# Kernel tuning notes

Hardware: AMD Instinct MI355X
Metric: run time of the kernel (lower is better)

The kernel has to match this reference:

```python
import jax, jax.numpy as jnp
import numpy as np

N_ = 512   # batch / num users
M_ = 254   # num UAV nodes -> size S = M_ + 2 = 256
D_ = 2     # coordinate dim
H_ = 128   # pointer-net hidden dim


def setup_inputs() -> dict:
    key = jax.random.key(0)
    ks = jax.random.split(key, 7)
    s = 0.1
    return {
        "outputs": jax.random.normal(ks[0], (2 * N_ + M_, D_), dtype=jnp.float32),
        "W_embed": jax.random.normal(ks[1], (D_, H_), dtype=jnp.float32) * s,
        "b_embed": jnp.zeros((H_,), jnp.float32),
        "lstm_Wi": jax.random.normal(ks[2], (H_, 4 * H_), dtype=jnp.float32) * s,
        "lstm_Wh": jax.random.normal(ks[3], (H_, 4 * H_), dtype=jnp.float32) * s,
        "lstm_b": jnp.zeros((4 * H_,), jnp.float32),
        "att_W1": jax.random.normal(ks[4], (H_, H_), dtype=jnp.float32) * s,
        "att_W2": jax.random.normal(ks[5], (H_, H_), dtype=jnp.float32) * s,
        "att_v": jax.random.normal(ks[6], (H_,), dtype=jnp.float32) * s,
        "N": N_,
    }


def _rgnn_loss(outputs, W_embed, b_embed, lstm_Wi, lstm_Wh, lstm_b,
               att_W1, att_W2, att_v, N):
    D = outputs.shape[1]
    H = W_embed.shape[1]
    M = outputs.shape[0] - 2 * N
    users_src = outputs[:N][:, None, :]                         # (B,1,D)
    users_dst = outputs[N:2 * N][:, None, :]                    # (B,1,D)
    uav_nodes = jnp.broadcast_to(outputs[2 * N:][None, :, :], (N, M, D))
    uav_graph = jnp.concatenate([users_src, uav_nodes, users_dst], axis=1)  # (B,S,D)
    B, S = uav_graph.shape[0], uav_graph.shape[1]
    NEG = jnp.float32(-np.inf)

    # pointer-net: node embeddings and step-independent attention projection
    e_all = uav_graph @ W_embed + b_embed                       # (B,S,H)
    W1e = jnp.einsum('bsh,hk->bsk', e_all, att_W1)              # (B,S,H)
    rows = jnp.arange(B)

    mask0 = jnp.zeros((B, S), jnp.float32).at[:, 0].set(NEG)
    x0 = uav_graph[:, 0, :]                                     # start at src
    carry0 = (x0, x0,
              jnp.zeros((B, H), jnp.float32), jnp.zeros((B, H), jnp.float32),
              mask0, jnp.zeros((B,), jnp.float32))

    def step(carry, k):
        x, Y0, h, c, mask, max_dist = carry
        # dst node blocked only at step 0, re-opened afterwards
        mask = mask.at[:, -1].set(jnp.where(k == 0, NEG, 0.0))
        # LSTM cell on embedded current node
        e_x = x @ W_embed + b_embed                             # (B,H)
        gates = e_x @ lstm_Wi + h @ lstm_Wh + lstm_b            # (B,4H)
        i, f, g, o = jnp.split(gates, 4, axis=1)
        c = jax.nn.sigmoid(f) * c + jax.nn.sigmoid(i) * jnp.tanh(g)
        h = jax.nn.sigmoid(o) * jnp.tanh(c)
        # additive attention pointer logits
        q = h @ att_W2                                          # (B,H)
        logits = jnp.tanh(W1e + q[:, None, :]) @ att_v + mask   # (B,S)
        logits = jax.lax.stop_gradient(logits)                  # output.detach()
        idx = jnp.argmax(logits, axis=1)                        # (B,)
        Y1 = uav_graph[rows, idx]                               # (B,D)
        dist = jnp.sqrt(jnp.sum((Y1 - Y0) ** 2, axis=1) + 1e-12)
        max_dist = jnp.maximum(max_dist, dist)
        mask = mask.at[rows, idx].add(NEG)
        mask = jnp.where((idx == S)[:, None], NEG, mask)
        return (Y1, Y1, h, c, mask, max_dist), None

    (_, _, _, _, _, max_dist), _ = jax.lax.scan(step, carry0, jnp.arange(S))
    return max_dist.mean()


def reference(outputs, W_embed, b_embed, lstm_Wi, lstm_Wh, lstm_b,
              att_W1, att_W2, att_v, N):
    return _rgnn_loss(outputs, W_embed, b_embed, lstm_Wi, lstm_Wh, lstm_b,
                      att_W1, att_W2, att_v, N)
```

## Files before the change

kernel.cpp:

```cpp
#include <hip/hip_runtime.h>
#include <math.h>

#define NB   512
#define MM   254
#define SS   256
#define HH   128
#define RTOT 1278
#define NBLK 256

#define C2   2.885390081777927f
#define C1   1.442695040888963f

__device__ __forceinline__ float rcpf(float x)  { return __builtin_amdgcn_rcpf(x); }
__device__ __forceinline__ float exp2f_(float x){ return __builtin_amdgcn_exp2f(x); }
__device__ __forceinline__ float sigm2(float x) { return rcpf(1.0f + exp2f_(-C1 * x)); }
__device__ __forceinline__ float tanh2(float x) { return 1.0f - 2.0f * rcpf(1.0f + exp2f_(C2 * x)); }

__global__ __launch_bounds__(512) void coef_k(
    const float* __restrict__ Wemb, const float* __restrict__ bemb,
    const float* __restrict__ Wi, const float* __restrict__ W1,
    const float* __restrict__ lb, float* __restrict__ coef)
{
  int j = threadIdx.x;
  float a = 0.f, b = 0.f, c = 0.f;
#pragma unroll 8
  for (int h = 0; h < HH; ++h) {
    float w = Wi[(size_t)h * 512 + j];
    a = fmaf(Wemb[h], w, a);
    b = fmaf(Wemb[HH + h], w, b);
    c = fmaf(bemb[h], w, c);
  }
  coef[j] = a; coef[512 + j] = b; coef[1024 + j] = c + lb[j];
  if (j < HH) {
    float a1 = 0.f, b1 = 0.f, c1 = 0.f;
#pragma unroll 8
    for (int h = 0; h < HH; ++h) {
      float w = W1[(size_t)h * HH + j];
      a1 = fmaf(Wemb[h], w, a1);
      b1 = fmaf(Wemb[HH + h], w, b1);
      c1 = fmaf(bemb[h], w, c1);
    }
    coef[1536 + j] = C2 * a1; coef[1664 + j] = C2 * b1; coef[1792 + j] = C2 * c1;
  }
}

__global__ __launch_bounds__(128) void transpose_k(
    const float* __restrict__ Wh, const float* __restrict__ W2,
    float* __restrict__ WhT, float* __restrict__ W2T)
{
  int bidx = blockIdx.x;
  int k = threadIdx.x;
  if (bidx < 512) WhT[(size_t)bidx * 128 + k] = Wh[(size_t)k * 512 + bidx];
  else {
    int j = bidx - 512;
    W2T[(size_t)j * 128 + k] = W2[(size_t)k * 128 + j];
  }
}

__global__ __attribute__((amdgpu_waves_per_eu(4, 4)))
__launch_bounds__(1024) void decode_k(
    const float* __restrict__ outputs, const float* __restrict__ WhT,
    const float* __restrict__ Wh, const float* __restrict__ W2T,
    const float* __restrict__ av, const float* __restrict__ coef,
    float* __restrict__ maxd_out)
{
  const int t = threadIdx.x;
  const int bid = blockIdx.x;

  __shared__ float WhL[64][512];
  __shared__ float posU[2 * MM];
  __shared__ float dstS[2][2];
  __shared__ float curP[2][2];
  __shared__ __align__(16) float hS[2][HH];
  __shared__ __align__(16) float qC[2][HH];
  __shared__ float C1sS[HH];
  __shared__ __align__(16) float A1sS[HH], B1sS[HH], vS2[HH];
  __shared__ __align__(16) float AiS[512], BiS[512], CiS[512];
  __shared__ float pS[2][2][512];
  __shared__ float lp[2][4][SS];
  __shared__ int   actS[2][254];
  __shared__ int   cntS[2];

  const int gh  = (t >> 5) & 1;
  const int gj  = ((t >> 6) << 5) | (t & 31);
  const int cg  = t >> 9;
  const int cj  = (t >> 2) & 127;
  const int ckq = t & 3;
  const int lg  = t >> 9;
  const int lhq = (t >> 7) & 3;
  const int lu  = t & 127;

  for (int i = t; i < 64 * 512; i += 1024) ((float*)WhL)[i] = Wh[64 * 512 + i];
  for (int i = t; i < 2 * MM; i += 1024)   posU[i] = outputs[4 * NB + i];
  if (t < HH) {
    C1sS[t] = coef[1792 + t];
    A1sS[t] = coef[1536 + t];
    B1sS[t] = coef[1664 + t];
    vS2[t]  = -2.0f * av[t];
  }
  if (t < 512) { AiS[t] = coef[t]; BiS[t] = coef[512 + t]; CiS[t] = coef[1024 + t]; }
  if (t < 256) { int gg = t >> 7, j = t & 127; hS[gg][j] = 0.f; }
  if (t < 254) actS[0][t] = t + 1;
  else if (t >= 512 && t < 766) actS[1][t - 512] = t - 511;
  if (t == 0) {
    cntS[0] = 254;
    dstS[0][0] = outputs[2 * (NB + bid)]; dstS[0][1] = outputs[2 * (NB + bid) + 1];
    curP[0][0] = outputs[2 * bid];        curP[0][1] = outputs[2 * bid + 1];
  }
  if (t == 512) {
    cntS[1] = 254;
    dstS[1][0] = outputs[2 * (NB + bid + NBLK)];
    dstS[1][1] = outputs[2 * (NB + bid + NBLK) + 1];
    curP[1][0] = outputs[2 * (bid + NBLK)];
    curP[1][1] = outputs[2 * (bid + NBLK) + 1];
  }
  __syncthreads();

  float px = 0.f, py = 0.f, md = 0.f;
  if (t == 0)   { px = curP[0][0]; py = curP[0][1]; }
  if (t == 512) { px = curP[1][0]; py = curP[1][1]; }

  float creg = 0.f;

  for (int k = 0; k < SS; ++k) {
    {
      const float4* wg4 = (const float4*)(WhT + (size_t)gj * 128 + gh * 32);
      const float*  wl  = &WhL[gh * 32][gj];
      const float4* hb0g = (const float4*)(&hS[0][gh * 32]);
      const float4* hb1g = (const float4*)(&hS[1][gh * 32]);
      const float4* hb0l = (const float4*)(&hS[0][64 + gh * 32]);
      const float4* hb1l = (const float4*)(&hS[1][64 + gh * 32]);
      float a0G = 0.f, a1G = 0.f, a0L = 0.f, a1L = 0.f;
      float4 wb[4];
#pragma unroll
      for (int i = 0; i < 4; ++i) wb[i] = wg4[i];
#pragma unroll
      for (int i = 0; i < 4; ++i) {
        float4 h0 = hb0l[i], h1 = hb1l[i];
        float wa = wl[(size_t)(4 * i) * 512];
        float wbv = wl[(size_t)(4 * i + 1) * 512];
        float wc = wl[(size_t)(4 * i + 2) * 512];
        float wd = wl[(size_t)(4 * i + 3) * 512];
        a0L = fmaf(h0.x, wa, a0L); a0L = fmaf(h0.y, wbv, a0L);
        a0L = fmaf(h0.z, wc, a0L); a0L = fmaf(h0.w, wd, a0L);
        a1L = fmaf(h1.x, wa, a1L); a1L = fmaf(h1.y, wbv, a1L);
        a1L = fmaf(h1.z, wc, a1L); a1L = fmaf(h1.w, wd, a1L);
      }
#pragma unroll
      for (int i = 0; i < 4; ++i) {
        float4 h0 = hb0g[i], h1 = hb1g[i], w = wb[i];
        a0G = fmaf(h0.x, w.x, a0G); a0G = fmaf(h0.y, w.y, a0G);
        a0G = fmaf(h0.z, w.z, a0G); a0G = fmaf(h0.w, w.w, a0G);
        a1G = fmaf(h1.x, w.x, a1G); a1G = fmaf(h1.y, w.y, a1G);
        a1G = fmaf(h1.z, w.z, a1G); a1G = fmaf(h1.w, w.w, a1G);
      }
#pragma unroll
      for (int i = 0; i < 4; ++i) wb[i] = wg4[4 + i];
#pragma unroll
      for (int i = 4; i < 8; ++i) {
        float4 h0 = hb0l[i], h1 = hb1l[i];
        float wa = wl[(size_t)(4 * i) * 512];
        float wbv = wl[(size_t)(4 * i + 1) * 512];
        float wc = wl[(size_t)(4 * i + 2) * 512];
        float wd = wl[(size_t)(4 * i + 3) * 512];
        a0L = fmaf(h0.x, wa, a0L); a0L = fmaf(h0.y, wbv, a0L);
        a0L = fmaf(h0.z, wc, a0L); a0L = fmaf(h0.w, wd, a0L);
        a1L = fmaf(h1.x, wa, a1L); a1L = fmaf(h1.y, wbv, a1L);
        a1L = fmaf(h1.z, wc, a1L); a1L = fmaf(h1.w, wd, a1L);
      }
#pragma unroll
      for (int i = 0; i < 4; ++i) {
        float4 h0 = hb0g[4 + i], h1 = hb1g[4 + i], w = wb[i];
        a0G = fmaf(h0.x, w.x, a0G); a0G = fmaf(h0.y, w.y, a0G);
        a0G = fmaf(h0.z, w.z, a0G); a0G = fmaf(h0.w, w.w, a0G);
        a1G = fmaf(h1.x, w.x, a1G); a1G = fmaf(h1.y, w.y, a1G);
        a1G = fmaf(h1.z, w.z, a1G); a1G = fmaf(h1.w, w.w, a1G);
      }
      pS[0][gh][gj] = a0G + a0L;
      pS[1][gh][gj] = a1G + a1L;
    }
    __syncthreads();

    if (t < 256) {
      int g = t >> 7, jj = t & 127;
      float pxc = curP[g][0], pyc = curP[g][1];
      float ei = fmaf(pxc, AiS[jj],       fmaf(pyc, BiS[jj],       CiS[jj]))       + (pS[g][0][jj]       + pS[g][1][jj]);
      float ef = fmaf(pxc, AiS[128 + jj], fmaf(pyc, BiS[128 + jj], CiS[128 + jj])) + (pS[g][0][128 + jj] + pS[g][1][128 + jj]);
      float eg2 = fmaf(pxc, AiS[256 + jj], fmaf(pyc, BiS[256 + jj], CiS[256 + jj])) + (pS[g][0][256 + jj] + pS[g][1][256 + jj]);
      float eo = fmaf(pxc, AiS[384 + jj], fmaf(pyc, BiS[384 + jj], CiS[384 + jj])) + (pS[g][0][384 + jj] + pS[g][1][384 + jj]);
      float iv = sigm2(ei), fv = sigm2(ef), gv = tanh2(eg2), ov = sigm2(eo);
      float cn = fv * creg + iv * gv;
      creg = cn;
      hS[g][jj] = ov * tanh2(cn);
    }
    __syncthreads();

    {
      const float4* w4 = (const float4*)(W2T + (size_t)cj * 128 + ckq * 32);
      const float4* h4 = (const float4*)(&hS[cg][ckq * 32]);
      float p0 = 0.f, p1 = 0.f;
#pragma unroll
      for (int i = 0; i < 8; ++i) {
        float4 w = w4[i], h = h4[i];
        p0 = fmaf(h.x, w.x, p0); p1 = fmaf(h.y, w.y, p1);
        p0 = fmaf(h.z, w.z, p0); p1 = fmaf(h.w, w.w, p1);
      }
      float p = p0 + p1;
      p += __shfl_xor(p, 1);
      p += __shfl_xor(p, 2);
      if (ckq == 0) qC[cg][cj] = fmaf(C2, p, C1sS[cj]);
    }
    __syncthreads();

    {
      int cnt = cntS[lg];
      int cntEff = cnt + (k > 0 ? 1 : 0);
      int u0 = lu, u1 = lu + 128;
      bool e0 = u0 < cntEff, e1 = u1 < cntEff;
      float px0 = 0.f, py0 = 0.f, px1 = 0.f, py1 = 0.f;
      if (e0) {
        int s0 = (u0 == cnt) ? 255 : actS[lg][u0];
        if (s0 == 255) { px0 = dstS[lg][0]; py0 = dstS[lg][1]; }
        else           { px0 = posU[2 * (s0 - 1)]; py0 = posU[2 * (s0 - 1) + 1]; }
      }
      if (e1) {
        int s1 = (u1 == cnt) ? 255 : actS[lg][u1];
        if (s1 == 255) { px1 = dstS[lg][0]; py1 = dstS[lg][1]; }
        else           { px1 = posU[2 * (s1 - 1)]; py1 = posU[2 * (s1 - 1) + 1]; }
      }
      const float4* a14 = (const float4*)(&A1sS[lhq * 32]);
      const float4* b14 = (const float4*)(&B1sS[lhq * 32]);
      const float4* qc4 = (const float4*)(&qC[lg][lhq * 32]);
      const float4* vv4 = (const float4*)(&vS2[lhq * 32]);
      float c00 = 0.f, c01 = 0.f, c10 = 0.f, c11 = 0.f;
#pragma unroll 4
      for (int i = 0; i < 8; ++i) {
        float4 a = a14[i], b = b14[i], qc = qc4[i], v = vv4[i];
        if (e0) {
          c00 = fmaf(v.x, rcpf(1.0f + exp2f_(fmaf(px0, a.x, fmaf(py0, b.x, qc.x)))), c00);
          c01 = fmaf(v.y, rcpf(1.0f + exp2f_(fmaf(px0, a.y, fmaf(py0, b.y, qc.y)))), c01);
          c00 = fmaf(v.z, rcpf(1.0f + exp2f_(fmaf(px0, a.z, fmaf(py0, b.z, qc.z)))), c00);
          c01 = fmaf(v.w, rcpf(1.0f + exp2f_(fmaf(px0, a.w, fmaf(py0, b.w, qc.w)))), c01);
        }
        if (e1) {
          c10 = fmaf(v.x, rcpf(1.0f + exp2f_(fmaf(px1, a.x, fmaf(py1, b.x, qc.x)))), c10);
          c11 = fmaf(v.y, rcpf(1.0f + exp2f_(fmaf(px1, a.y, fmaf(py1, b.y, qc.y)))), c11);
          c10 = fmaf(v.z, rcpf(1.0f + exp2f_(fmaf(px1, a.z, fmaf(py1, b.z, qc.z)))), c10);
          c11 = fmaf(v.w, rcpf(1.0f + exp2f_(fmaf(px1, a.w, fmaf(py1, b.w, qc.w)))), c11);
        }
      }
      if (e0) lp[lg][lhq][u0] = c00 + c01;
      if (e1) lp[lg][lhq][u1] = c10 + c11;
    }
    __syncthreads();

    if ((t < 64) || (t >= 512 && t < 576)) {
      int g = t >> 9;
      int lane = t & 63;
      int cnt = cntS[g];
      int cntEff = cnt + (k > 0 ? 1 : 0);
      float val = -INFINITY;
      unsigned key = 0xFFFFFFFFu;
#pragma unroll 2
      for (int c = 0; c < 4; ++c) {
        int u = lane + 64 * c;
        if (u < cntEff) {
          float v2 = (lp[g][0][u] + lp[g][1][u]) + (lp[g][2][u] + lp[g][3][u]);
          int s = (u == cnt) ? 255 : actS[g][u];
          unsigned k2 = ((unsigned)s << 16) | (unsigned)u;
          if (v2 > val || (v2 == val && k2 < key)) { val = v2; key = k2; }
        }
      }
#pragma unroll
      for (int off = 1; off < 64; off <<= 1) {
        float v2 = __shfl_xor(val, off);
        unsigned k2 = __shfl_xor(key, off);
        if (v2 > val || (v2 == val && k2 < key)) { val = v2; key = k2; }
      }
      if (lane == 0) {
        int s   = (int)(key >> 16);
        int pos = (int)(key & 0xFFFFu);
        float nx, ny;
        if (s == 255) { nx = dstS[g][0]; ny = dstS[g][1]; }
        else          { nx = posU[2 * (s - 1)]; ny = posU[2 * (s - 1) + 1]; }
        float dx = nx - px, dy = ny - py;
        float d = sqrtf(dx * dx + dy * dy + 1e-12f);
        if (d > md) md = d;
        px = nx; py = ny;
        curP[g][0] = nx; curP[g][1] = ny;
        if (s != 255) { actS[g][pos] = actS[g][cnt - 1]; cntS[g] = cnt - 1; }
      }
    }
    __syncthreads();
  }

  if (t == 0)   maxd_out[bid] = md;
  if (t == 512) maxd_out[bid + NBLK] = md;
}

__global__ __launch_bounds__(512) void reduce_k(const float* __restrict__ maxd,
                                               float* __restrict__ out)
{
  __shared__ float s[512];
  int t = threadIdx.x;
  s[t] = maxd[t];
  __syncthreads();
  for (int off = 256; off > 0; off >>= 1) {
    if (t < off) s[t] += s[t + off];
    __syncthreads();
  }
  if (t == 0) out[0] = s[0] * (1.0f / 512.0f);
}

extern "C" void kernel_launch(void* const* d_in, const int* in_sizes, int n_in,
                              void* d_out, int out_size, void* d_ws, size_t ws_size,
                              hipStream_t stream) {
  const float* outputs = (const float*)d_in[0];
  const float* Wemb    = (const float*)d_in[1];
  const float* bemb    = (const float*)d_in[2];
  const float* Wi      = (const float*)d_in[3];
  const float* Wh      = (const float*)d_in[4];
  const float* lb      = (const float*)d_in[5];
  const float* W1      = (const float*)d_in[6];
  const float* W2      = (const float*)d_in[7];
  const float* av      = (const float*)d_in[8];

  float* ws   = (float*)d_ws;
  float* coef = ws;
  float* WhT  = coef + 2048;
  float* W2T  = WhT + (size_t)512 * 128;
  float* maxd = W2T + (size_t)128 * 128;

  hipLaunchKernelGGL(coef_k, dim3(1), dim3(512), 0, stream,
                     Wemb, bemb, Wi, W1, lb, coef);
  hipLaunchKernelGGL(transpose_k, dim3(640), dim3(128), 0, stream, Wh, W2, WhT, W2T);
  hipLaunchKernelGGL(decode_k, dim3(NBLK), dim3(1024), 0, stream,
                     outputs, WhT, Wh, W2T, av, coef, maxd);
  hipLaunchKernelGGL(reduce_k, dim3(1), dim3(512), 0, stream, maxd, (float*)d_out);
}
```

Before: 2.122 ms.

## Stagger two per-block teams by two phases to overlap decode stages

The decode kernel now gives each 512-thread half of the block its own batch element, so each half computes its full gate matvec instead of the two halves splitting the work across both elements. The second team starts two phases behind the first, so the five phases (gate matvec, LSTM update, query projection, attention logits, argmax) of the two teams run in a staggered pipeline. This is meant to mix different instruction types on the CU at the same moment and avoid whole-block idle time in the lightly occupied phases. In exchange there are two extra stage barriers, per-thread dot products are twice as long, and each team reads the full Wh matrix on its own.

After: 7.943 ms. 3.74x slower.

```diff
diff --git a/kernel.cpp b/kernel.cpp
--- a/kernel.cpp
+++ b/kernel.cpp
@@ -66,6 +66,9 @@
 {
   const int t = threadIdx.x;
   const int bid = blockIdx.x;
+  const int team  = t >> 9;
+  const int local = t & 511;
+  const int g = team;
 
   __shared__ float WhL[64][512];
   __shared__ float posU[2 * MM];
@@ -76,19 +79,15 @@
   __shared__ float C1sS[HH];
   __shared__ __align__(16) float A1sS[HH], B1sS[HH], vS2[HH];
   __shared__ __align__(16) float AiS[512], BiS[512], CiS[512];
-  __shared__ float pS[2][2][512];
+  __shared__ __align__(16) float gS[2][512];
   __shared__ float lp[2][4][SS];
   __shared__ int   actS[2][254];
   __shared__ int   cntS[2];
 
-  const int gh  = (t >> 5) & 1;
-  const int gj  = ((t >> 6) << 5) | (t & 31);
-  const int cg  = t >> 9;
-  const int cj  = (t >> 2) & 127;
-  const int ckq = t & 3;
-  const int lg  = t >> 9;
-  const int lhq = (t >> 7) & 3;
-  const int lu  = t & 127;
+  const int cj  = (local >> 2) & 127;
+  const int ckq = local & 3;
+  const int lhq = (local >> 7) & 3;
+  const int lu  = local & 127;
 
   for (int i = t; i < 64 * 512; i += 1024) ((float*)WhL)[i] = Wh[64 * 512 + i];
   for (int i = t; i < 2 * MM; i += 1024)   posU[i] = outputs[4 * NB + i];
@@ -117,185 +116,161 @@
   __syncthreads();
 
   float px = 0.f, py = 0.f, md = 0.f;
-  if (t == 0)   { px = curP[0][0]; py = curP[0][1]; }
-  if (t == 512) { px = curP[1][0]; py = curP[1][1]; }
+  if (local == 0) {
+    int b = bid + (g << 8);
+    px = outputs[2 * b]; py = outputs[2 * b + 1];
+  }
 
   float creg = 0.f;
 
-  for (int k = 0; k < SS; ++k) {
-    {
-      const float4* wg4 = (const float4*)(WhT + (size_t)gj * 128 + gh * 32);
-      const float*  wl  = &WhL[gh * 32][gj];
-      const float4* hb0g = (const float4*)(&hS[0][gh * 32]);
-      const float4* hb1g = (const float4*)(&hS[1][gh * 32]);
-      const float4* hb0l = (const float4*)(&hS[0][64 + gh * 32]);
-      const float4* hb1l = (const float4*)(&hS[1][64 + gh * 32]);
-      float a0G = 0.f, a1G = 0.f, a0L = 0.f, a1L = 0.f;
-      float4 wb[4];
-#pragma unroll
-      for (int i = 0; i < 4; ++i) wb[i] = wg4[i];
-#pragma unroll
-      for (int i = 0; i < 4; ++i) {
-        float4 h0 = hb0l[i], h1 = hb1l[i];
-        float wa = wl[(size_t)(4 * i) * 512];
-        float wbv = wl[(size_t)(4 * i + 1) * 512];
-        float wc = wl[(size_t)(4 * i + 2) * 512];
-        float wd = wl[(size_t)(4 * i + 3) * 512];
-        a0L = fmaf(h0.x, wa, a0L); a0L = fmaf(h0.y, wbv, a0L);
-        a0L = fmaf(h0.z, wc, a0L); a0L = fmaf(h0.w, wd, a0L);
-        a1L = fmaf(h1.x, wa, a1L); a1L = fmaf(h1.y, wbv, a1L);
-        a1L = fmaf(h1.z, wc, a1L); a1L = fmaf(h1.w, wd, a1L);
-      }
-#pragma unroll
-      for (int i = 0; i < 4; ++i) {
-        float4 h0 = hb0g[i], h1 = hb1g[i], w = wb[i];
-        a0G = fmaf(h0.x, w.x, a0G); a0G = fmaf(h0.y, w.y, a0G);
-        a0G = fmaf(h0.z, w.z, a0G); a0G = fmaf(h0.w, w.w, a0G);
-        a1G = fmaf(h1.x, w.x, a1G); a1G = fmaf(h1.y, w.y, a1G);
-        a1G = fmaf(h1.z, w.z, a1G); a1G = fmaf(h1.w, w.w, a1G);
-      }
-#pragma unroll
-      for (int i = 0; i < 4; ++i) wb[i] = wg4[4 + i];
-#pragma unroll
-      for (int i = 4; i < 8; ++i) {
-        float4 h0 = hb0l[i], h1 = hb1l[i];
-        float wa = wl[(size_t)(4 * i) * 512];
-        float wbv = wl[(size_t)(4 * i + 1) * 512];
-        float wc = wl[(size_t)(4 * i + 2) * 512];
-        float wd = wl[(size_t)(4 * i + 3) * 512];
-        a0L = fmaf(h0.x, wa, a0L); a0L = fmaf(h0.y, wbv, a0L);
-        a0L = fmaf(h0.z, wc, a0L); a0L = fmaf(h0.w, wd, a0L);
-        a1L = fmaf(h1.x, wa, a1L); a1L = fmaf(h1.y, wbv, a1L);
-        a1L = fmaf(h1.z, wc, a1L); a1L = fmaf(h1.w, wd, a1L);
-      }
-#pragma unroll
-      for (int i = 0; i < 4; ++i) {
-        float4 h0 = hb0g[4 + i], h1 = hb1g[4 + i], w = wb[i];
-        a0G = fmaf(h0.x, w.x, a0G); a0G = fmaf(h0.y, w.y, a0G);
-        a0G = fmaf(h0.z, w.z, a0G); a0G = fmaf(h0.w, w.w, a0G);
-        a1G = fmaf(h1.x, w.x, a1G); a1G = fmaf(h1.y, w.y, a1G);
-        a1G = fmaf(h1.z, w.z, a1G); a1G = fmaf(h1.w, w.w, a1G);
-      }
-      pS[0][gh][gj] = a0G + a0L;
-      pS[1][gh][gj] = a1G + a1L;
-    }
-    __syncthreads();
-
-    if (t < 256) {
-      int g = t >> 7, jj = t & 127;
-      float pxc = curP[g][0], pyc = curP[g][1];
-      float ei = fmaf(pxc, AiS[jj],       fmaf(pyc, BiS[jj],       CiS[jj]))       + (pS[g][0][jj]       + pS[g][1][jj]);
-      float ef = fmaf(pxc, AiS[128 + jj], fmaf(pyc, BiS[128 + jj], CiS[128 + jj])) + (pS[g][0][128 + jj] + pS[g][1][128 + jj]);
-      float eg2 = fmaf(pxc, AiS[256 + jj], fmaf(pyc, BiS[256 + jj], CiS[256 + jj])) + (pS[g][0][256 + jj] + pS[g][1][256 + jj]);
-      float eo = fmaf(pxc, AiS[384 + jj], fmaf(pyc, BiS[384 + jj], CiS[384 + jj])) + (pS[g][0][384 + jj] + pS[g][1][384 + jj]);
-      float iv = sigm2(ei), fv = sigm2(ef), gv = tanh2(eg2), ov = sigm2(eo);
-      float cn = fv * creg + iv * gv;
-      creg = cn;
-      hS[g][jj] = ov * tanh2(cn);
-    }
-    __syncthreads();
-
-    {
-      const float4* w4 = (const float4*)(W2T + (size_t)cj * 128 + ckq * 32);
-      const float4* h4 = (const float4*)(&hS[cg][ckq * 32]);
-      float p0 = 0.f, p1 = 0.f;
-#pragma unroll
-      for (int i = 0; i < 8; ++i) {
-        float4 w = w4[i], h = h4[i];
-        p0 = fmaf(h.x, w.x, p0); p1 = fmaf(h.y, w.y, p1);
-        p0 = fmaf(h.z, w.z, p0); p1 = fmaf(h.w, w.w, p1);
-      }
-      float p = p0 + p1;
-      p += __shfl_xor(p, 1);
-      p += __shfl_xor(p, 2);
-      if (ckq == 0) qC[cg][cj] = fmaf(C2, p, C1sS[cj]);
-    }
-    __syncthreads();
-
-    {
-      int cnt = cntS[lg];
-      int cntEff = cnt + (k > 0 ? 1 : 0);
-      int u0 = lu, u1 = lu + 128;
-      bool e0 = u0 < cntEff, e1 = u1 < cntEff;
-      float px0 = 0.f, py0 = 0.f, px1 = 0.f, py1 = 0.f;
-      if (e0) {
-        int s0 = (u0 == cnt) ? 255 : actS[lg][u0];
-        if (s0 == 255) { px0 = dstS[lg][0]; py0 = dstS[lg][1]; }
-        else           { px0 = posU[2 * (s0 - 1)]; py0 = posU[2 * (s0 - 1) + 1]; }
-      }
-      if (e1) {
-        int s1 = (u1 == cnt) ? 255 : actS[lg][u1];
-        if (s1 == 255) { px1 = dstS[lg][0]; py1 = dstS[lg][1]; }
-        else           { px1 = posU[2 * (s1 - 1)]; py1 = posU[2 * (s1 - 1) + 1]; }
-      }
-      const float4* a14 = (const float4*)(&A1sS[lhq * 32]);
-      const float4* b14 = (const float4*)(&B1sS[lhq * 32]);
-      const float4* qc4 = (const float4*)(&qC[lg][lhq * 32]);
-      const float4* vv4 = (const float4*)(&vS2[lhq * 32]);
-      float c00 = 0.f, c01 = 0.f, c10 = 0.f, c11 = 0.f;
+  int ph = (team == 0) ? 0 : -2;
+  int lk = 0;
+
+  const int NSTAGE = 5 * SS + 2;
+  for (int sg = 0; sg < NSTAGE; ++sg) {
+    bool valid = (ph >= 0) && (lk < SS);
+    if (valid) {
+      if (ph == 0) {
+        int j = local;
+        const float4* wg4 = (const float4*)(WhT + (size_t)j * 128);
+        const float*  wl  = &WhL[0][j];
+        const float4* hg4 = (const float4*)(&hS[g][0]);
+        const float4* hl4 = (const float4*)(&hS[g][64]);
+        float aG = 0.f, aG2 = 0.f, aL = 0.f, aL2 = 0.f;
+#pragma unroll
+        for (int b = 0; b < 4; ++b) {
+          float4 wb[4];
+#pragma unroll
+          for (int i = 0; i < 4; ++i) wb[i] = wg4[b * 4 + i];
+#pragma unroll
+          for (int i = 0; i < 4; ++i) {
+            float4 h = hg4[b * 4 + i];
+            aG  = fmaf(h.x, wb[i].x, aG);  aG2 = fmaf(h.y, wb[i].y, aG2);
+            aG  = fmaf(h.z, wb[i].z, aG);  aG2 = fmaf(h.w, wb[i].w, aG2);
+          }
+        }
 #pragma unroll 4
-      for (int i = 0; i < 8; ++i) {
-        float4 a = a14[i], b = b14[i], qc = qc4[i], v = vv4[i];
+        for (int i = 0; i < 16; ++i) {
+          float4 h = hl4[i];
+          float w0 = wl[(size_t)(4 * i + 0) * 512];
+          float w1 = wl[(size_t)(4 * i + 1) * 512];
+          float w2 = wl[(size_t)(4 * i + 2) * 512];
+          float w3 = wl[(size_t)(4 * i + 3) * 512];
+          aL  = fmaf(h.x, w0, aL);  aL2 = fmaf(h.y, w1, aL2);
+          aL  = fmaf(h.z, w2, aL);  aL2 = fmaf(h.w, w3, aL2);
+        }
+        gS[g][j] = (aG + aG2) + (aL + aL2);
+      } else if (ph == 1) {
+        if (local < 128) {
+          int jj = local;
+          float pxc = curP[g][0], pyc = curP[g][1];
+          float ei = fmaf(pxc, AiS[jj],       fmaf(pyc, BiS[jj],       CiS[jj]))       + gS[g][jj];
+          float ef = fmaf(pxc, AiS[128 + jj], fmaf(pyc, BiS[128 + jj], CiS[128 + jj])) + gS[g][128 + jj];
+          float eg2 = fmaf(pxc, AiS[256 + jj], fmaf(pyc, BiS[256 + jj], CiS[256 + jj])) + gS[g][256 + jj];
+          float eo = fmaf(pxc, AiS[384 + jj], fmaf(pyc, BiS[384 + jj], CiS[384 + jj])) + gS[g][384 + jj];
+          float iv = sigm2(ei), fv = sigm2(ef), gv = tanh2(eg2), ov = sigm2(eo);
+          float cn = fv * creg + iv * gv;
+          creg = cn;
+          hS[g][jj] = ov * tanh2(cn);
+        }
+      } else if (ph == 2) {
+        const float4* w4 = (const float4*)(W2T + (size_t)cj * 128 + ckq * 32);
+        const float4* h4 = (const float4*)(&hS[g][ckq * 32]);
+        float p0 = 0.f, p1 = 0.f;
+#pragma unroll
+        for (int i = 0; i < 8; ++i) {
+          float4 w = w4[i], h = h4[i];
+          p0 = fmaf(h.x, w.x, p0); p1 = fmaf(h.y, w.y, p1);
+          p0 = fmaf(h.z, w.z, p0); p1 = fmaf(h.w, w.w, p1);
+        }
+        float p = p0 + p1;
+        p += __shfl_xor(p, 1);
+        p += __shfl_xor(p, 2);
+        if (ckq == 0) qC[g][cj] = fmaf(C2, p, C1sS[cj]);
+      } else if (ph == 3) {
+        int cnt = cntS[g];
+        int cntEff = cnt + (lk > 0 ? 1 : 0);
+        int u0 = lu, u1 = lu + 128;
+        bool e0 = u0 < cntEff, e1 = u1 < cntEff;
+        float px0 = 0.f, py0 = 0.f, px1 = 0.f, py1 = 0.f;
         if (e0) {
-          c00 = fmaf(v.x, rcpf(1.0f + exp2f_(fmaf(px0, a.x, fmaf(py0, b.x, qc.x)))), c00);
-          c01 = fmaf(v.y, rcpf(1.0f + exp2f_(fmaf(px0, a.y, fmaf(py0, b.y, qc.y)))), c01);
-          c00 = fmaf(v.z, rcpf(1.0f + exp2f_(fmaf(px0, a.z, fmaf(py0, b.z, qc.z)))), c00);
-          c01 = fmaf(v.w, rcpf(1.0f + exp2f_(fmaf(px0, a.w, fmaf(py0, b.w, qc.w)))), c01);
+          int s0 = (u0 == cnt) ? 255 : actS[g][u0];
+          if (s0 == 255) { px0 = dstS[g][0]; py0 = dstS[g][1]; }
+          else           { px0 = posU[2 * (s0 - 1)]; py0 = posU[2 * (s0 - 1) + 1]; }
         }
         if (e1) {
-          c10 = fmaf(v.x, rcpf(1.0f + exp2f_(fmaf(px1, a.x, fmaf(py1, b.x, qc.x)))), c10);
-          c11 = fmaf(v.y, rcpf(1.0f + exp2f_(fmaf(px1, a.y, fmaf(py1, b.y, qc.y)))), c11);
-          c10 = fmaf(v.z, rcpf(1.0f + exp2f_(fmaf(px1, a.z, fmaf(py1, b.z, qc.z)))), c10);
-          c11 = fmaf(v.w, rcpf(1.0f + exp2f_(fmaf(px1, a.w, fmaf(py1, b.w, qc.w)))), c11);
-        }
-      }
-      if (e0) lp[lg][lhq][u0] = c00 + c01;
-      if (e1) lp[lg][lhq][u1] = c10 + c11;
-    }
-    __syncthreads();
-
-    if ((t < 64) || (t >= 512 && t < 576)) {
-      int g = t >> 9;
-      int lane = t & 63;
-      int cnt = cntS[g];
-      int cntEff = cnt + (k > 0 ? 1 : 0);
-      float val = -INFINITY;
-      unsigned key = 0xFFFFFFFFu;
+          int s1 = (u1 == cnt) ? 255 : actS[g][u1];
+          if (s1 == 255) { px1 = dstS[g][0]; py1 = dstS[g][1]; }
+          else           { px1 = posU[2 * (s1 - 1)]; py1 = posU[2 * (s1 - 1) + 1]; }
+        }
+        const float4* a14 = (const float4*)(&A1sS[lhq * 32]);
+        const float4* b14 = (const float4*)(&B1sS[lhq * 32]);
+        const float4* qc4 = (const float4*)(&qC[g][lhq * 32]);
+        const float4* vv4 = (const float4*)(&vS2[lhq * 32]);
+        float c00 = 0.f, c01 = 0.f, c10 = 0.f, c11 = 0.f;
+#pragma unroll 4
+        for (int i = 0; i < 8; ++i) {
+          float4 a = a14[i], b = b14[i], qc = qc4[i], v = vv4[i];
+          if (e0) {
+            c00 = fmaf(v.x, rcpf(1.0f + exp2f_(fmaf(px0, a.x, fmaf(py0, b.x, qc.x)))), c00);
+            c01 = fmaf(v.y, rcpf(1.0f + exp2f_(fmaf(px0, a.y, fmaf(py0, b.y, qc.y)))), c01);
+            c00 = fmaf(v.z, rcpf(1.0f + exp2f_(fmaf(px0, a.z, fmaf(py0, b.z, qc.z)))), c00);
+            c01 = fmaf(v.w, rcpf(1.0f + exp2f_(fmaf(px0, a.w, fmaf(py0, b.w, qc.w)))), c01);
+          }
+          if (e1) {
+            c10 = fmaf(v.x, rcpf(1.0f + exp2f_(fmaf(px1, a.x, fmaf(py1, b.x, qc.x)))), c10);
+            c11 = fmaf(v.y, rcpf(1.0f + exp2f_(fmaf(px1, a.y, fmaf(py1, b.y, qc.y)))), c11);
+            c10 = fmaf(v.z, rcpf(1.0f + exp2f_(fmaf(px1, a.z, fmaf(py1, b.z, qc.z)))), c10);
+            c11 = fmaf(v.w, rcpf(1.0f + exp2f_(fmaf(px1, a.w, fmaf(py1, b.w, qc.w)))), c11);
+          }
+        }
+        if (e0) lp[g][lhq][u0] = c00 + c01;
+        if (e1) lp[g][lhq][u1] = c10 + c11;
+      } else {
+        if (local < 64) {
+          int lane = local;
+          int cnt = cntS[g];
+          int cntEff = cnt + (lk > 0 ? 1 : 0);
+          float val = -INFINITY;
+          unsigned key = 0xFFFFFFFFu;
 #pragma unroll 2
-      for (int c = 0; c < 4; ++c) {
-        int u = lane + 64 * c;
-        if (u < cntEff) {
-          float v2 = (lp[g][0][u] + lp[g][1][u]) + (lp[g][2][u] + lp[g][3][u]);
-          int s = (u == cnt) ? 255 : actS[g][u];
-          unsigned k2 = ((unsigned)s << 16) | (unsigned)u;
-          if (v2 > val || (v2 == val && k2 < key)) { val = v2; key = k2; }
-        }
-      }
-#pragma unroll
-      for (int off = 1; off < 64; off <<= 1) {
-        float v2 = __shfl_xor(val, off);
-        unsigned k2 = __shfl_xor(key, off);
-        if (v2 > val || (v2 == val && k2 < key)) { val = v2; key = k2; }
-      }
-      if (lane == 0) {
-        int s   = (int)(key >> 16);
-        int pos = (int)(key & 0xFFFFu);
-        float nx, ny;
-        if (s == 255) { nx = dstS[g][0]; ny = dstS[g][1]; }
-        else          { nx = posU[2 * (s - 1)]; ny = posU[2 * (s - 1) + 1]; }
-        float dx = nx - px, dy = ny - py;
-        float d = sqrtf(dx * dx + dy * dy + 1e-12f);
-        if (d > md) md = d;
-        px = nx; py = ny;
-        curP[g][0] = nx; curP[g][1] = ny;
-        if (s != 255) { actS[g][pos] = actS[g][cnt - 1]; cntS[g] = cnt - 1; }
+          for (int c = 0; c < 4; ++c) {
+            int u = lane + 64 * c;
+            if (u < cntEff) {
+              float v2 = (lp[g][0][u] + lp[g][1][u]) + (lp[g][2][u] + lp[g][3][u]);
+              int s = (u == cnt) ? 255 : actS[g][u];
+              unsigned k2 = ((unsigned)s << 16) | (unsigned)u;
+              if (v2 > val || (v2 == val && k2 < key)) { val = v2; key = k2; }
+            }
+          }
+#pragma unroll
+          for (int off = 1; off < 64; off <<= 1) {
+            float v2 = __shfl_xor(val, off);
+            unsigned k2 = __shfl_xor(key, off);
+            if (v2 > val || (v2 == val && k2 < key)) { val = v2; key = k2; }
+          }
+          if (lane == 0) {
+            int s   = (int)(key >> 16);
+            int pos = (int)(key & 0xFFFFu);
+            float nx, ny;
+            if (s == 255) { nx = dstS[g][0]; ny = dstS[g][1]; }
+            else          { nx = posU[2 * (s - 1)]; ny = posU[2 * (s - 1) + 1]; }
+            float dx = nx - px, dy = ny - py;
+            float d = sqrtf(dx * dx + dy * dy + 1e-12f);
+            if (d > md) md = d;
+            px = nx; py = ny;
+            curP[g][0] = nx; curP[g][1] = ny;
+            if (s != 255) { actS[g][pos] = actS[g][cnt - 1]; cntS[g] = cnt - 1; }
+          }
+        }
       }
     }
+    ++ph;
+    if (ph == 5) { ph = 0; ++lk; }
     __syncthreads();
   }
 
-  if (t == 0)   maxd_out[bid] = md;
-  if (t == 512) maxd_out[bid + NBLK] = md;
+  if (local == 0) maxd_out[bid + (g << 8)] = md;
 }
 
 __global__ __launch_bounds__(512) void reduce_k(const float* __restrict__ maxd,
```
